# Kernel tuning notes

Measured on AMD Instinct MI355X. Metric: run time of the kernel, lower is better.

The kernel has to match this reference:

```python
import jax, jax.numpy as jnp
import numpy as np

N_NODES = 100000
N_EDGES = 1600000
D_IN = 128
D_HID = 128
N_CLASSES = 40


def _glorot(key, fan_in, fan_out):
    lim = np.sqrt(6.0 / (fan_in + fan_out)).astype(np.float32)
    return jax.random.uniform(key, (fan_in, fan_out), jnp.float32, -lim, lim)


def setup_inputs() -> dict:
    key = jax.random.key(0)
    ks = jax.random.split(key, 10)
    x = jax.random.normal(ks[0], (N_NODES, D_IN), jnp.float32)
    edge_index = jax.random.randint(ks[1], (2, N_EDGES), 0, N_NODES, jnp.int64)
    return {
        "x": x,
        "edge_index": edge_index,
        # layer 1: lin_l (neighbor, with bias), lin_r (root, no bias)
        "W1l": _glorot(ks[2], D_IN, D_HID),
        "b1": jnp.zeros((D_HID,), jnp.float32),
        "W1r": _glorot(ks[3], D_IN, D_HID),
        # layer 2
        "W2l": _glorot(ks[4], D_HID, D_HID),
        "b2": jnp.zeros((D_HID,), jnp.float32),
        "W2r": _glorot(ks[5], D_HID, D_HID),
        # layer 3
        "W3l": _glorot(ks[6], D_HID, N_CLASSES),
        "b3": jnp.zeros((N_CLASSES,), jnp.float32),
        "W3r": _glorot(ks[7], D_HID, N_CLASSES),
    }


def _sage_conv(x, src, dst, deg_inv, Wl, bl, Wr):
    # mean aggregation of source-node features onto destination nodes
    msgs = x[src]                                            # [E, d] gather
    agg = jax.ops.segment_sum(msgs, dst, num_segments=N_NODES)  # [N, d]
    agg = agg * deg_inv[:, None]                             # mean
    return agg @ Wl + bl + x @ Wr


def reference(x, edge_index, W1l, b1, W1r, W2l, b2, W2r, W3l, b3, W3r):
    src, dst = edge_index[0], edge_index[1]
    deg = jax.ops.segment_sum(jnp.ones((N_EDGES,), x.dtype), dst,
                              num_segments=N_NODES)
    deg_inv = 1.0 / jnp.maximum(deg, 1.0)
    h = _sage_conv(x, src, dst, deg_inv, W1l, b1, W1r)
    h = jax.nn.relu(h)  # dropout is identity in eval mode
    h = _sage_conv(h, src, dst, deg_inv, W2l, b2, W2r)
    h = jax.nn.relu(h)
    h = _sage_conv(h, src, dst, deg_inv, W3l, b3, W3r)
    return jax.nn.log_softmax(h, axis=1)
```

## Files before the change

kernel.cpp:

```cpp
#include <hip/hip_runtime.h>
#include <math.h>

#define D 128
#define NCLS 40
#define NBLK_P1 256

typedef unsigned int u32;
typedef __attribute__((ext_vector_type(8))) short short8;
typedef __attribute__((ext_vector_type(4))) float f32x4;

__device__ inline float bflo(u32 u){ return __uint_as_float(u << 16); }
__device__ inline float bfhi(u32 u){ return __uint_as_float(u & 0xffff0000u); }
__device__ inline u32 pack2bf(float a, float b){
  u32 ua = __float_as_uint(a), ub = __float_as_uint(b);
  ua += 0x7fffu + ((ua >> 16) & 1u);
  ub += 0x7fffu + ((ub >> 16) & 1u);
  return (ua >> 16) | (ub & 0xffff0000u);
}
__device__ inline unsigned short pack1bf(float a){
  u32 ua = __float_as_uint(a);
  ua += 0x7fffu + ((ua >> 16) & 1u);
  return (unsigned short)(ua >> 16);
}

__global__ __launch_bounds__(256) void prep_k(
    const float4* __restrict__ x4, uint2* __restrict__ xb, int n4,
    const float* __restrict__ W1l, const float* __restrict__ W1r, u32* __restrict__ Wt1,
    const float* __restrict__ W2l, const float* __restrict__ W2r, u32* __restrict__ Wt2,
    const float* __restrict__ W3l, const float* __restrict__ W3r,
    u32* __restrict__ Wt3b, float* __restrict__ bias3b, const float* __restrict__ b3,
    const int* __restrict__ dst, int* __restrict__ gcnt, int E, int nbuk, int nbX)
{
  __shared__ int cnt[1024];
  const int b = blockIdx.x;
  const int tid = threadIdx.x;
  if (b < nbX){
    int i = b * 256 + tid;
    if (i < n4){
      float4 v = x4[i];
      xb[i] = make_uint2(pack2bf(v.x, v.y), pack2bf(v.z, v.w));
    }
  } else if (b < nbX + 128){
    const bool first = (b < nbX + 64);
    const float* Wl = first ? W1l : W2l;
    const float* Wr = first ? W1r : W2r;
    u32* Wt = first ? Wt1 : Wt2;
    int i = ((b - nbX) & 63) * 256 + tid;
    int nn = i >> 7, kp = i & 127;
    int k = kp * 2;
    float a, c;
    if (k < 128){ a = Wl[(size_t)k * 128 + nn]; c = Wl[(size_t)(k + 1) * 128 + nn]; }
    else        { a = Wr[(size_t)(k - 128) * 128 + nn]; c = Wr[(size_t)(k - 127) * 128 + nn]; }
    Wt[(size_t)nn * 128 + kp] = pack2bf(a, c);
  } else if (b < nbX + 160){
    int i = (b - nbX - 128) * 256 + tid;
    if (i < 128 * 64){
      int nn = i >> 6, kp = i & 63;
      int k = kp * 2;
      float a = 0.f, c = 0.f;
      if (nn < NCLS){
        a = W3l[(size_t)k * NCLS + nn]; c = W3l[(size_t)(k + 1) * NCLS + nn];
      } else if (nn >= 64 && nn < 64 + NCLS){
        int cc = nn - 64;
        a = W3r[(size_t)k * NCLS + cc]; c = W3r[(size_t)(k + 1) * NCLS + cc];
      }
      Wt3b[(size_t)nn * 64 + kp] = pack2bf(a, c);
    }
    if (b == nbX + 128 && tid < 128)
      bias3b[tid] = (tid >= 64 && tid < 64 + NCLS) ? b3[tid - 64] : 0.f;
  } else {
    const int hb = b - nbX - 160;
    for (int i = tid; i < nbuk; i += 256) cnt[i] = 0;
    __syncthreads();
    const int per = (E + NBLK_P1 - 1) / NBLK_P1;
    const int e0 = hb * per;
    const int e1 = min(e0 + per, E);
    for (int i = e0 + tid; i < e1; i += 256)
      atomicAdd(&cnt[dst[i] >> 7], 1);
    __syncthreads();
    for (int i = tid; i < nbuk; i += 256)
      gcnt[(size_t)hb * nbuk + i] = cnt[i];
  }
}


__global__ __launch_bounds__(1024) void part_scan_k(
    const int* __restrict__ gcnt, int* __restrict__ goff,
    int* __restrict__ bbase, int nbuk)
{
  __shared__ int sm[1024];
  const int j = threadIdx.x;
  int btot = 0;
  if (j < nbuk)
    for (int i = 0; i < NBLK_P1; i++) btot += gcnt[(size_t)i * nbuk + j];
  sm[j] = btot;
  __syncthreads();
  int acc = btot;
  for (int off = 1; off < 1024; off <<= 1){
    int t = (j >= off) ? sm[j - off] : 0;
    __syncthreads();
    acc += t; sm[j] = acc;
    __syncthreads();
  }
  const int base = acc - btot;
  if (j < nbuk){
    bbase[j] = base;
    if (j == nbuk - 1) bbase[nbuk] = base + btot;
    int run = base;
    for (int i = 0; i < NBLK_P1; i++){
      goff[(size_t)i * nbuk + j] = run;
      run += gcnt[(size_t)i * nbuk + j];
    }
  }
}

__global__ __launch_bounds__(256) void part_fill_k(
    const int* __restrict__ src, const int* __restrict__ dst,
    const int* __restrict__ goff, u32* __restrict__ staging,
    int E, int nbuk)
{
  __shared__ int boff[1024];
  __shared__ int cur[1024];
  const int tid = threadIdx.x;
  for (int i = tid; i < nbuk; i += 256){
    boff[i] = goff[(size_t)blockIdx.x * nbuk + i];
    cur[i] = 0;
  }
  __syncthreads();
  const int per = (E + NBLK_P1 - 1) / NBLK_P1;
  const int e0 = blockIdx.x * per;
  const int e1 = min(e0 + per, E);
  for (int i = e0 + tid; i < e1; i += 256){
    int d = dst[i];
    int s = src[i];
    int b = d >> 7;
    int p = atomicAdd(&cur[b], 1);
    staging[boff[b] + p] = ((u32)s << 7) | (u32)(d & 127);
  }
}

__global__ __launch_bounds__(256) void bucket_csr_k(
    const u32* __restrict__ staging, const int* __restrict__ bbase,
    int* __restrict__ csr_off, float* __restrict__ deg_inv,
    int* __restrict__ csr_src, int N)
{
  __shared__ int ldeg[128];
  __shared__ int sm[128];
  __shared__ int lbase[128];
  __shared__ int lpos[128];
  const int b = blockIdx.x;
  const int node0 = b << 7;
  const int tid = threadIdx.x;
  if (tid < 128) ldeg[tid] = 0;
  __syncthreads();
  const int lo = bbase[b], hi = bbase[b + 1];
  for (int i = lo + tid; i < hi; i += 256)
    atomicAdd(&ldeg[staging[i] & 127u], 1);
  __syncthreads();
  if (tid < 128) sm[tid] = ldeg[tid];
  __syncthreads();
  for (int off = 1; off < 128; off <<= 1){
    int t = (tid >= off && tid < 128) ? sm[tid - off] : 0;
    __syncthreads();
    if (tid < 128) sm[tid] += t;
    __syncthreads();
  }
  if (tid < 128){
    const int excl = sm[tid] - ldeg[tid];
    lbase[tid] = lo + excl;
    lpos[tid] = 0;
    const int node = node0 + tid;
    if (node < N){
      csr_off[node] = lo + excl;
      deg_inv[node] = 1.0f / fmaxf((float)ldeg[tid], 1.0f);
    } else if (node == N){
      csr_off[N] = lo + excl;
    }
  }
  if (tid == 0 && b == (int)gridDim.x - 1) csr_off[N] = hi;
  __syncthreads();
  for (int i = lo + tid; i < hi; i += 256){
    u32 v = staging[i];
    int dloc = (int)(v & 127u);
    int p = atomicAdd(&lpos[dloc], 1);
    csr_src[lbase[dloc] + p] = (int)(v >> 7);
  }
}

__device__ inline void add8(float* acc, uint4 v){
  acc[0] += bflo(v.x); acc[1] += bfhi(v.x);
  acc[2] += bflo(v.y); acc[3] += bfhi(v.y);
  acc[4] += bflo(v.z); acc[5] += bfhi(v.z);
  acc[6] += bflo(v.w); acc[7] += bfhi(v.w);
}

__global__ __launch_bounds__(256) void aggregate_k(
    const u32* __restrict__ feat, const int* __restrict__ coff,
    const int* __restrict__ csr_src, const float* __restrict__ deg_inv,
    u32* __restrict__ agg, int n)
{
  const int g = threadIdx.x >> 4;
  const int lane = threadIdx.x & 15;
  const int node = blockIdx.x * 16 + g;
  if (node >= n) return;
  const int lo = coff[node], hi = coff[node + 1];
  const uint4* __restrict__ f4 = (const uint4*)feat;
  float acc[8] = {0.f,0.f,0.f,0.f,0.f,0.f,0.f,0.f};
  int e = lo;
  for (; e + 7 < hi; e += 8){
    int s0 = csr_src[e],     s1 = csr_src[e + 1];
    int s2 = csr_src[e + 2], s3 = csr_src[e + 3];
    int s4 = csr_src[e + 4], s5 = csr_src[e + 5];
    int s6 = csr_src[e + 6], s7 = csr_src[e + 7];
    uint4 v0 = f4[(size_t)s0 * 16 + lane];
    uint4 v1 = f4[(size_t)s1 * 16 + lane];
    uint4 v2 = f4[(size_t)s2 * 16 + lane];
    uint4 v3 = f4[(size_t)s3 * 16 + lane];
    uint4 v4 = f4[(size_t)s4 * 16 + lane];
    uint4 v5 = f4[(size_t)s5 * 16 + lane];
    uint4 v6 = f4[(size_t)s6 * 16 + lane];
    uint4 v7 = f4[(size_t)s7 * 16 + lane];
    add8(acc, v0); add8(acc, v1); add8(acc, v2); add8(acc, v3);
    add8(acc, v4); add8(acc, v5); add8(acc, v6); add8(acc, v7);
  }
  for (; e + 3 < hi; e += 4){
    int s0 = csr_src[e],     s1 = csr_src[e + 1];
    int s2 = csr_src[e + 2], s3 = csr_src[e + 3];
    uint4 v0 = f4[(size_t)s0 * 16 + lane];
    uint4 v1 = f4[(size_t)s1 * 16 + lane];
    uint4 v2 = f4[(size_t)s2 * 16 + lane];
    uint4 v3 = f4[(size_t)s3 * 16 + lane];
    add8(acc, v0); add8(acc, v1); add8(acc, v2); add8(acc, v3);
  }
  for (; e < hi; ++e){
    uint4 v0 = f4[(size_t)csr_src[e] * 16 + lane];
    add8(acc, v0);
  }
  const float di = deg_inv[node];
  uint4 o;
  o.x = pack2bf(acc[0] * di, acc[1] * di);
  o.y = pack2bf(acc[2] * di, acc[3] * di);
  o.z = pack2bf(acc[4] * di, acc[5] * di);
  o.w = pack2bf(acc[6] * di, acc[7] * di);
  ((uint4*)agg)[(size_t)node * 16 + lane] = o;
}

__global__ __launch_bounds__(256) void gemm_mfma_k(
    const u32* __restrict__ A1, const u32* __restrict__ A2,
    const u32* __restrict__ Wt, const float* __restrict__ bias,
    u32* __restrict__ out, int n)
{
  __shared__ u32 As_u[128 * 20];
  __shared__ u32 Bs_u[128 * 20];
  const int tid = threadIdx.x;
  const int row0 = blockIdx.x * 128;
  const int l = tid & 63, w = tid >> 6;
  const int lm = l & 15, lq = l >> 4;

  f32x4 acc[2][8];
  #pragma unroll
  for (int mi = 0; mi < 2; mi++)
    #pragma unroll
    for (int ni = 0; ni < 8; ni++) acc[mi][ni] = (f32x4){0.f, 0.f, 0.f, 0.f};

  for (int kt = 0; kt < 8; ++kt){
    const u32* Ap = (kt < 4) ? A1 : A2;
    const int ko = (kt & 3) * 16;
    #pragma unroll
    for (int i = 0; i < 2; i++){
      int chunk = tid + 256 * i;
      int row = chunk >> 2, q = chunk & 3;
      uint4 av = make_uint4(0, 0, 0, 0);
      int gr = row0 + row;
      if (gr < n) av = *(const uint4*)(Ap + (size_t)gr * 64 + ko + q * 4);
      *(uint4*)&As_u[row * 20 + q * 4] = av;
      uint4 bv = *(const uint4*)(Wt + (size_t)row * 128 + kt * 16 + q * 4);
      *(uint4*)&Bs_u[row * 20 + q * 4] = bv;
    }
    __syncthreads();
    short8 af0 = *(const short8*)&As_u[(w * 32 + lm) * 20 + lq * 4];
    short8 af1 = *(const short8*)&As_u[(w * 32 + 16 + lm) * 20 + lq * 4];
    #pragma unroll
    for (int ni = 0; ni < 8; ni++){
      short8 bf = *(const short8*)&Bs_u[(ni * 16 + lm) * 20 + lq * 4];
      acc[0][ni] = __builtin_amdgcn_mfma_f32_16x16x32_bf16(af0, bf, acc[0][ni], 0, 0, 0);
      acc[1][ni] = __builtin_amdgcn_mfma_f32_16x16x32_bf16(af1, bf, acc[1][ni], 0, 0, 0);
    }
    __syncthreads();
  }

  float bb[8];
  #pragma unroll
  for (int ni = 0; ni < 8; ni++) bb[ni] = bias[ni * 16 + lm];
  unsigned short* outp = (unsigned short*)out;
  #pragma unroll
  for (int mi = 0; mi < 2; mi++){
    #pragma unroll
    for (int r = 0; r < 4; r++){
      int row = row0 + w * 32 + mi * 16 + lq * 4 + r;
      if (row < n){
        #pragma unroll
        for (int ni = 0; ni < 8; ni++){
          float v = fmaxf(acc[mi][ni][r] + bb[ni], 0.f);
          outp[(size_t)row * 128 + ni * 16 + lm] = pack1bf(v);
        }
      }
    }
  }
}

__global__ __launch_bounds__(256) void gemm3_mfma_k(
    const u32* __restrict__ A, const u32* __restrict__ Wt3b,
    const float* __restrict__ bias, u32* __restrict__ out, int n)
{
  __shared__ u32 As_u[128 * 20];
  __shared__ u32 Bs_u[128 * 20];
  const int tid = threadIdx.x;
  const int row0 = blockIdx.x * 128;
  const int l = tid & 63, w = tid >> 6;
  const int lm = l & 15, lq = l >> 4;

  f32x4 acc[2][8];
  #pragma unroll
  for (int mi = 0; mi < 2; mi++)
    #pragma unroll
    for (int ni = 0; ni < 8; ni++) acc[mi][ni] = (f32x4){0.f, 0.f, 0.f, 0.f};

  for (int kt = 0; kt < 4; ++kt){
    #pragma unroll
    for (int i = 0; i < 2; i++){
      int chunk = tid + 256 * i;
      int row = chunk >> 2, q = chunk & 3;
      uint4 av = make_uint4(0, 0, 0, 0);
      int gr = row0 + row;
      if (gr < n) av = *(const uint4*)(A + (size_t)gr * 64 + kt * 16 + q * 4);
      *(uint4*)&As_u[row * 20 + q * 4] = av;
      uint4 bv = *(const uint4*)(Wt3b + (size_t)row * 64 + kt * 16 + q * 4);
      *(uint4*)&Bs_u[row * 20 + q * 4] = bv;
    }
    __syncthreads();
    short8 af0 = *(const short8*)&As_u[(w * 32 + lm) * 20 + lq * 4];
    short8 af1 = *(const short8*)&As_u[(w * 32 + 16 + lm) * 20 + lq * 4];
    #pragma unroll
    for (int ni = 0; ni < 8; ni++){
      short8 bf = *(const short8*)&Bs_u[(ni * 16 + lm) * 20 + lq * 4];
      acc[0][ni] = __builtin_amdgcn_mfma_f32_16x16x32_bf16(af0, bf, acc[0][ni], 0, 0, 0);
      acc[1][ni] = __builtin_amdgcn_mfma_f32_16x16x32_bf16(af1, bf, acc[1][ni], 0, 0, 0);
    }
    __syncthreads();
  }

  float bb[8];
  #pragma unroll
  for (int ni = 0; ni < 8; ni++) bb[ni] = bias[ni * 16 + lm];
  unsigned short* outp = (unsigned short*)out;
  #pragma unroll
  for (int mi = 0; mi < 2; mi++){
    #pragma unroll
    for (int r = 0; r < 4; r++){
      int row = row0 + w * 32 + mi * 16 + lq * 4 + r;
      if (row < n){
        #pragma unroll
        for (int ni = 0; ni < 8; ni++){
          float v = acc[mi][ni][r] + bb[ni];
          outp[(size_t)row * 128 + ni * 16 + lm] = pack1bf(v);
        }
      }
    }
  }
}

__global__ __launch_bounds__(256) void agg_softmax_k(
    const u32* __restrict__ yz, const int* __restrict__ coff,
    const int* __restrict__ csr_src, const float* __restrict__ deg_inv,
    float* __restrict__ out, int n)
{
  const int g = threadIdx.x >> 3;
  const int lane = threadIdx.x & 7;
  const int node = blockIdx.x * 32 + g;
  if (node >= n) return;
  const int lo = coff[node], hi = coff[node + 1];
  const uint4* __restrict__ f4 = (const uint4*)yz;
  float acc[8] = {0.f,0.f,0.f,0.f,0.f,0.f,0.f,0.f};
  int e = lo;
  for (; e + 7 < hi; e += 8){
    int s0 = csr_src[e],     s1 = csr_src[e + 1];
    int s2 = csr_src[e + 2], s3 = csr_src[e + 3];
    int s4 = csr_src[e + 4], s5 = csr_src[e + 5];
    int s6 = csr_src[e + 6], s7 = csr_src[e + 7];
    uint4 v0 = f4[(size_t)s0 * 16 + lane];
    uint4 v1 = f4[(size_t)s1 * 16 + lane];
    uint4 v2 = f4[(size_t)s2 * 16 + lane];
    uint4 v3 = f4[(size_t)s3 * 16 + lane];
    uint4 v4 = f4[(size_t)s4 * 16 + lane];
    uint4 v5 = f4[(size_t)s5 * 16 + lane];
    uint4 v6 = f4[(size_t)s6 * 16 + lane];
    uint4 v7 = f4[(size_t)s7 * 16 + lane];
    add8(acc, v0); add8(acc, v1); add8(acc, v2); add8(acc, v3);
    add8(acc, v4); add8(acc, v5); add8(acc, v6); add8(acc, v7);
  }
  for (; e + 3 < hi; e += 4){
    int s0 = csr_src[e],     s1 = csr_src[e + 1];
    int s2 = csr_src[e + 2], s3 = csr_src[e + 3];
    uint4 v0 = f4[(size_t)s0 * 16 + lane];
    uint4 v1 = f4[(size_t)s1 * 16 + lane];
    uint4 v2 = f4[(size_t)s2 * 16 + lane];
    uint4 v3 = f4[(size_t)s3 * 16 + lane];
    add8(acc, v0); add8(acc, v1); add8(acc, v2); add8(acc, v3);
  }
  for (; e < hi; ++e){
    uint4 v0 = f4[(size_t)csr_src[e] * 16 + lane];
    add8(acc, v0);
  }
  const float di = deg_inv[node];
  uint4 zv = f4[(size_t)node * 16 + 8 + lane];
  float v[8];
  v[0] = acc[0] * di + bflo(zv.x); v[1] = acc[1] * di + bfhi(zv.x);
  v[2] = acc[2] * di + bflo(zv.y); v[3] = acc[3] * di + bfhi(zv.y);
  v[4] = acc[4] * di + bflo(zv.z); v[5] = acc[5] * di + bfhi(zv.z);
  v[6] = acc[6] * di + bflo(zv.w); v[7] = acc[7] * di + bfhi(zv.w);
  const bool valid = (lane < 5);
  float m = -INFINITY;
  if (valid){
    #pragma unroll
    for (int j = 0; j < 8; j++) m = fmaxf(m, v[j]);
  }
  #pragma unroll
  for (int off = 1; off < 8; off <<= 1) m = fmaxf(m, __shfl_xor(m, off, 64));
  float s = 0.f;
  if (valid){
    #pragma unroll
    for (int j = 0; j < 8; j++) s += __expf(v[j] - m);
  }
  #pragma unroll
  for (int off = 1; off < 8; off <<= 1) s += __shfl_xor(s, off, 64);
  const float ls = m + logf(s);
  if (valid){
    float* op = out + (size_t)node * NCLS + lane * 8;
    *(float4*)op     = make_float4(v[0]-ls, v[1]-ls, v[2]-ls, v[3]-ls);
    *(float4*)(op+4) = make_float4(v[4]-ls, v[5]-ls, v[6]-ls, v[7]-ls);
  }
}


extern "C" void kernel_launch(void* const* d_in, const int* in_sizes, int n_in,
                              void* d_out, int out_size, void* d_ws, size_t ws_size,
                              hipStream_t stream) {
  const float* x   = (const float*)d_in[0];
  const int*   ei  = (const int*)d_in[1];
  const float* W1l = (const float*)d_in[2];
  const float* b1  = (const float*)d_in[3];
  const float* W1r = (const float*)d_in[4];
  const float* W2l = (const float*)d_in[5];
  const float* b2  = (const float*)d_in[6];
  const float* W2r = (const float*)d_in[7];
  const float* W3l = (const float*)d_in[8];
  const float* b3  = (const float*)d_in[9];
  const float* W3r = (const float*)d_in[10];

  const int N = in_sizes[0] / D;
  const int E = in_sizes[1] / 2;
  const int* src = ei;
  const int* dst = ei + E;
  const int nbuk = (N + 127) >> 7;

  char* ws = (char*)d_ws;
  auto alloc = [&](size_t bytes) -> void* {
    void* p = (void*)ws;
    ws += (bytes + 255) & ~(size_t)255;
    return p;
  };
  int*   csr_off  = (int*)  alloc((size_t)(N + 1) * 4);
  float* deg_inv  = (float*)alloc((size_t)N * 4);
  int*   csr_src  = (int*)  alloc((size_t)E * 4);
  u32*   staging  = (u32*)  alloc((size_t)E * 4);
  int*   gcnt     = (int*)  alloc((size_t)NBLK_P1 * nbuk * 4);
  int*   goff     = (int*)  alloc((size_t)NBLK_P1 * nbuk * 4);
  int*   bbase    = (int*)  alloc((size_t)(nbuk + 1) * 4);
  u32*   xb       = (u32*)  alloc((size_t)N * D * 2);
  u32*   agg      = (u32*)  alloc((size_t)N * D * 2);
  u32*   hbuf     = (u32*)  alloc((size_t)N * D * 2);
  u32*   yz       = (u32*)  alloc((size_t)N * D * 2);
  u32*   Wt1      = (u32*)  alloc((size_t)128 * 128 * 4);
  u32*   Wt2      = (u32*)  alloc((size_t)128 * 128 * 4);
  u32*   Wt3b    = (u32*)  alloc((size_t)128 * 64 * 4);
  float* bias3b   = (float*)alloc((size_t)128 * 4);

  const int n4 = N * D / 4;
  const int nbX = (n4 + 255) / 256;
  prep_k<<<nbX + 160 + NBLK_P1, 256, 0, stream>>>(
      (const float4*)x, (uint2*)xb, n4,
      W1l, W1r, Wt1, W2l, W2r, Wt2,
      W3l, W3r, Wt3b, bias3b, b3,
      dst, gcnt, E, nbuk, nbX);

  part_scan_k<<<1, 1024, 0, stream>>>(gcnt, goff, bbase, nbuk);
  part_fill_k<<<NBLK_P1, 256, 0, stream>>>(src, dst, goff, staging, E, nbuk);
  bucket_csr_k<<<nbuk, 256, 0, stream>>>(staging, bbase, csr_off, deg_inv, csr_src, N);

  const int gblocks = (N + 127) / 128;
  const int ablocks = (N + 15) / 16;
  aggregate_k<<<ablocks, 256, 0, stream>>>(xb, csr_off, csr_src, deg_inv, agg, N);
  gemm_mfma_k<<<gblocks, 256, 0, stream>>>(agg, xb, Wt1, b1, hbuf, N);
  aggregate_k<<<ablocks, 256, 0, stream>>>(hbuf, csr_off, csr_src, deg_inv, agg, N);
  gemm_mfma_k<<<gblocks, 256, 0, stream>>>(agg, hbuf, Wt2, b2, hbuf, N);
  gemm3_mfma_k<<<gblocks, 256, 0, stream>>>(hbuf, Wt3b, bias3b, yz, N);
  agg_softmax_k<<<(N + 31) / 32, 256, 0, stream>>>(yz, csr_off, csr_src, deg_inv,
                                                   (float*)d_out, N);
}
```

Before: 390.4 us.

## Store bf16 features column-chunked so gathers stay cache-resident per chunk

Features are stored in a chunk-major layout: eight 16-column bf16 chunks, each contiguous across all nodes. Aggregation kernels now process one chunk per block, so each pass gathers from a 3.2MB slab that can stay in cache instead of scattering across full 256B rows. Within a node, four lanes split the edges and are combined with shuffles. The final aggregate-plus-softmax is split into a chunked fp32 aggregation and a separate softmax kernel. The cost is an extra launch and an fp32 intermediate round trip, with more blocks each re-reading the CSR offsets and indices.

```diff
diff --git a/kernel.cpp b/kernel.cpp
--- a/kernel.cpp
+++ b/kernel.cpp
@@ -8,6 +8,7 @@
 typedef unsigned int u32;
 typedef __attribute__((ext_vector_type(8))) short short8;
 typedef __attribute__((ext_vector_type(4))) float f32x4;
+typedef __attribute__((ext_vector_type(4))) u32 u32x4;
 
 __device__ inline float bflo(u32 u){ return __uint_as_float(u << 16); }
 __device__ inline float bfhi(u32 u){ return __uint_as_float(u & 0xffff0000u); }
@@ -23,8 +24,9 @@
   return (unsigned short)(ua >> 16);
 }
 
+
 __global__ __launch_bounds__(256) void prep_k(
-    const float4* __restrict__ x4, uint2* __restrict__ xb, int n4,
+    const float4* __restrict__ x4, u32* __restrict__ xb, int n4,
     const float* __restrict__ W1l, const float* __restrict__ W1r, u32* __restrict__ Wt1,
     const float* __restrict__ W2l, const float* __restrict__ W2r, u32* __restrict__ Wt2,
     const float* __restrict__ W3l, const float* __restrict__ W3r,
@@ -37,8 +39,12 @@
   if (b < nbX){
     int i = b * 256 + tid;
     if (i < n4){
+      const int NN = n4 >> 5;
       float4 v = x4[i];
-      xb[i] = make_uint2(pack2bf(v.x, v.y), pack2bf(v.z, v.w));
+      int node = i >> 5;
+      int cu = (i * 2) & 63;
+      size_t idx = ((size_t)(cu >> 3) * NN + node) * 8 + (cu & 7);
+      *(uint2*)&xb[idx] = make_uint2(pack2bf(v.x, v.y), pack2bf(v.z, v.w));
     }
   } else if (b < nbX + 128){
     const bool first = (b < nbX + 64);
@@ -194,55 +200,48 @@
   acc[6] += bflo(v.w); acc[7] += bfhi(v.w);
 }
 
-__global__ __launch_bounds__(256) void aggregate_k(
+__global__ __launch_bounds__(256) void aggregate_c_k(
     const u32* __restrict__ feat, const int* __restrict__ coff,
     const int* __restrict__ csr_src, const float* __restrict__ deg_inv,
     u32* __restrict__ agg, int n)
 {
-  const int g = threadIdx.x >> 4;
-  const int lane = threadIdx.x & 15;
-  const int node = blockIdx.x * 16 + g;
+  const int c = blockIdx.x & 7;
+  const int g = threadIdx.x >> 3;
+  const int lane = threadIdx.x & 7;
+  const int node = (blockIdx.x >> 3) * 32 + g;
   if (node >= n) return;
+  const int h = lane & 1;
+  const int eslot = lane >> 1;
+  const uint4* __restrict__ Fc = (const uint4*)(feat + (size_t)c * n * 8);
   const int lo = coff[node], hi = coff[node + 1];
-  const uint4* __restrict__ f4 = (const uint4*)feat;
   float acc[8] = {0.f,0.f,0.f,0.f,0.f,0.f,0.f,0.f};
-  int e = lo;
-  for (; e + 7 < hi; e += 8){
-    int s0 = csr_src[e],     s1 = csr_src[e + 1];
-    int s2 = csr_src[e + 2], s3 = csr_src[e + 3];
-    int s4 = csr_src[e + 4], s5 = csr_src[e + 5];
-    int s6 = csr_src[e + 6], s7 = csr_src[e + 7];
-    uint4 v0 = f4[(size_t)s0 * 16 + lane];
-    uint4 v1 = f4[(size_t)s1 * 16 + lane];
-    uint4 v2 = f4[(size_t)s2 * 16 + lane];
-    uint4 v3 = f4[(size_t)s3 * 16 + lane];
-    uint4 v4 = f4[(size_t)s4 * 16 + lane];
-    uint4 v5 = f4[(size_t)s5 * 16 + lane];
-    uint4 v6 = f4[(size_t)s6 * 16 + lane];
-    uint4 v7 = f4[(size_t)s7 * 16 + lane];
-    add8(acc, v0); add8(acc, v1); add8(acc, v2); add8(acc, v3);
-    add8(acc, v4); add8(acc, v5); add8(acc, v6); add8(acc, v7);
-  }
-  for (; e + 3 < hi; e += 4){
-    int s0 = csr_src[e],     s1 = csr_src[e + 1];
-    int s2 = csr_src[e + 2], s3 = csr_src[e + 3];
-    uint4 v0 = f4[(size_t)s0 * 16 + lane];
-    uint4 v1 = f4[(size_t)s1 * 16 + lane];
-    uint4 v2 = f4[(size_t)s2 * 16 + lane];
-    uint4 v3 = f4[(size_t)s3 * 16 + lane];
-    add8(acc, v0); add8(acc, v1); add8(acc, v2); add8(acc, v3);
-  }
-  for (; e < hi; ++e){
-    uint4 v0 = f4[(size_t)csr_src[e] * 16 + lane];
+  int e = lo + eslot;
+  for (; e + 4 < hi; e += 8){
+    int s0 = __builtin_nontemporal_load(csr_src + e);
+    int s1 = __builtin_nontemporal_load(csr_src + e + 4);
+    uint4 v0 = Fc[(size_t)s0 * 2 + h];
+    uint4 v1 = Fc[(size_t)s1 * 2 + h];
+    add8(acc, v0); add8(acc, v1);
+  }
+  if (e < hi){
+    int s0 = __builtin_nontemporal_load(csr_src + e);
+    uint4 v0 = Fc[(size_t)s0 * 2 + h];
     add8(acc, v0);
   }
-  const float di = deg_inv[node];
-  uint4 o;
-  o.x = pack2bf(acc[0] * di, acc[1] * di);
-  o.y = pack2bf(acc[2] * di, acc[3] * di);
-  o.z = pack2bf(acc[4] * di, acc[5] * di);
-  o.w = pack2bf(acc[6] * di, acc[7] * di);
-  ((uint4*)agg)[(size_t)node * 16 + lane] = o;
+  #pragma unroll
+  for (int off = 2; off <= 4; off <<= 1)
+    #pragma unroll
+    for (int j = 0; j < 8; j++)
+      acc[j] += __shfl_xor(acc[j], off, 64);
+  if (eslot == 0){
+    const float di = deg_inv[node];
+    u32x4 o;
+    o.x = pack2bf(acc[0] * di, acc[1] * di);
+    o.y = pack2bf(acc[2] * di, acc[3] * di);
+    o.z = pack2bf(acc[4] * di, acc[5] * di);
+    o.w = pack2bf(acc[6] * di, acc[7] * di);
+    __builtin_nontemporal_store(o, (u32x4*)(agg + ((size_t)c * n + node) * 8 + h * 4));
+  }
 }
 
 __global__ __launch_bounds__(256) void gemm_mfma_k(
@@ -272,7 +271,8 @@
       int row = chunk >> 2, q = chunk & 3;
       uint4 av = make_uint4(0, 0, 0, 0);
       int gr = row0 + row;
-      if (gr < n) av = *(const uint4*)(Ap + (size_t)gr * 64 + ko + q * 4);
+      int cu = ko + q * 4;
+      if (gr < n) av = *(const uint4*)(Ap + ((size_t)(cu >> 3) * n + gr) * 8 + (cu & 7));
       *(uint4*)&As_u[row * 20 + q * 4] = av;
       uint4 bv = *(const uint4*)(Wt + (size_t)row * 128 + kt * 16 + q * 4);
       *(uint4*)&Bs_u[row * 20 + q * 4] = bv;
@@ -302,7 +302,7 @@
         #pragma unroll
         for (int ni = 0; ni < 8; ni++){
           float v = fmaxf(acc[mi][ni][r] + bb[ni], 0.f);
-          outp[(size_t)row * 128 + ni * 16 + lm] = pack1bf(v);
+          outp[((size_t)ni * n + row) * 16 + lm] = pack1bf(v);
         }
       }
     }
@@ -333,7 +333,8 @@
       int row = chunk >> 2, q = chunk & 3;
       uint4 av = make_uint4(0, 0, 0, 0);
       int gr = row0 + row;
-      if (gr < n) av = *(const uint4*)(A + (size_t)gr * 64 + kt * 16 + q * 4);
+      int cu = kt * 16 + q * 4;
+      if (gr < n) av = *(const uint4*)(A + ((size_t)(cu >> 3) * n + gr) * 8 + (cu & 7));
       *(uint4*)&As_u[row * 20 + q * 4] = av;
       uint4 bv = *(const uint4*)(Wt3b + (size_t)row * 64 + kt * 16 + q * 4);
       *(uint4*)&Bs_u[row * 20 + q * 4] = bv;
@@ -363,62 +364,74 @@
         #pragma unroll
         for (int ni = 0; ni < 8; ni++){
           float v = acc[mi][ni][r] + bb[ni];
-          outp[(size_t)row * 128 + ni * 16 + lm] = pack1bf(v);
+          outp[((size_t)ni * n + row) * 16 + lm] = pack1bf(v);
         }
       }
     }
   }
 }
 
-__global__ __launch_bounds__(256) void agg_softmax_k(
+__global__ __launch_bounds__(256) void yagg_c_k(
     const u32* __restrict__ yz, const int* __restrict__ coff,
     const int* __restrict__ csr_src, const float* __restrict__ deg_inv,
+    float* __restrict__ yagg, int n)
+{
+  const int c = blockIdx.x & 3;
+  const int g = threadIdx.x >> 3;
+  const int lane = threadIdx.x & 7;
+  const int node = (blockIdx.x >> 2) * 32 + g;
+  if (node >= n) return;
+  const int h = lane & 1;
+  const int eslot = lane >> 1;
+  const uint4* __restrict__ Fc = (const uint4*)(yz + (size_t)c * n * 8);
+  const int lo = coff[node], hi = coff[node + 1];
+  float acc[8] = {0.f,0.f,0.f,0.f,0.f,0.f,0.f,0.f};
+  int e = lo + eslot;
+  for (; e + 4 < hi; e += 8){
+    int s0 = __builtin_nontemporal_load(csr_src + e);
+    int s1 = __builtin_nontemporal_load(csr_src + e + 4);
+    uint4 v0 = Fc[(size_t)s0 * 2 + h];
+    uint4 v1 = Fc[(size_t)s1 * 2 + h];
+    add8(acc, v0); add8(acc, v1);
+  }
+  if (e < hi){
+    int s0 = __builtin_nontemporal_load(csr_src + e);
+    uint4 v0 = Fc[(size_t)s0 * 2 + h];
+    add8(acc, v0);
+  }
+  #pragma unroll
+  for (int off = 2; off <= 4; off <<= 1)
+    #pragma unroll
+    for (int j = 0; j < 8; j++)
+      acc[j] += __shfl_xor(acc[j], off, 64);
+  if (eslot == 0){
+    const float di = deg_inv[node];
+    float* yp = yagg + ((size_t)c * n + node) * 16 + h * 8;
+    f32x4 o0 = (f32x4){acc[0]*di, acc[1]*di, acc[2]*di, acc[3]*di};
+    f32x4 o1 = (f32x4){acc[4]*di, acc[5]*di, acc[6]*di, acc[7]*di};
+    __builtin_nontemporal_store(o0, (f32x4*)yp);
+    __builtin_nontemporal_store(o1, (f32x4*)(yp + 4));
+  }
+}
+
+__global__ __launch_bounds__(256) void softmax_k(
+    const float* __restrict__ yagg, const u32* __restrict__ yz,
     float* __restrict__ out, int n)
 {
   const int g = threadIdx.x >> 3;
   const int lane = threadIdx.x & 7;
   const int node = blockIdx.x * 32 + g;
   if (node >= n) return;
-  const int lo = coff[node], hi = coff[node + 1];
-  const uint4* __restrict__ f4 = (const uint4*)yz;
-  float acc[8] = {0.f,0.f,0.f,0.f,0.f,0.f,0.f,0.f};
-  int e = lo;
-  for (; e + 7 < hi; e += 8){
-    int s0 = csr_src[e],     s1 = csr_src[e + 1];
-    int s2 = csr_src[e + 2], s3 = csr_src[e + 3];
-    int s4 = csr_src[e + 4], s5 = csr_src[e + 5];
-    int s6 = csr_src[e + 6], s7 = csr_src[e + 7];
-    uint4 v0 = f4[(size_t)s0 * 16 + lane];
-    uint4 v1 = f4[(size_t)s1 * 16 + lane];
-    uint4 v2 = f4[(size_t)s2 * 16 + lane];
-    uint4 v3 = f4[(size_t)s3 * 16 + lane];
-    uint4 v4 = f4[(size_t)s4 * 16 + lane];
-    uint4 v5 = f4[(size_t)s5 * 16 + lane];
-    uint4 v6 = f4[(size_t)s6 * 16 + lane];
-    uint4 v7 = f4[(size_t)s7 * 16 + lane];
-    add8(acc, v0); add8(acc, v1); add8(acc, v2); add8(acc, v3);
-    add8(acc, v4); add8(acc, v5); add8(acc, v6); add8(acc, v7);
-  }
-  for (; e + 3 < hi; e += 4){
-    int s0 = csr_src[e],     s1 = csr_src[e + 1];
-    int s2 = csr_src[e + 2], s3 = csr_src[e + 3];
-    uint4 v0 = f4[(size_t)s0 * 16 + lane];
-    uint4 v1 = f4[(size_t)s1 * 16 + lane];
-    uint4 v2 = f4[(size_t)s2 * 16 + lane];
-    uint4 v3 = f4[(size_t)s3 * 16 + lane];
-    add8(acc, v0); add8(acc, v1); add8(acc, v2); add8(acc, v3);
-  }
-  for (; e < hi; ++e){
-    uint4 v0 = f4[(size_t)csr_src[e] * 16 + lane];
-    add8(acc, v0);
-  }
-  const float di = deg_inv[node];
-  uint4 zv = f4[(size_t)node * 16 + 8 + lane];
+  const float4* yp = (const float4*)(yagg + ((size_t)(lane >> 1) * n + node) * 16
+                                     + (lane & 1) * 8);
+  float4 a0 = yp[0], a1 = yp[1];
+  const uint4 zv = *(const uint4*)(yz + ((size_t)(4 + (lane >> 1)) * n + node) * 8
+                                   + (lane & 1) * 4);
   float v[8];
-  v[0] = acc[0] * di + bflo(zv.x); v[1] = acc[1] * di + bfhi(zv.x);
-  v[2] = acc[2] * di + bflo(zv.y); v[3] = acc[3] * di + bfhi(zv.y);
-  v[4] = acc[4] * di + bflo(zv.z); v[5] = acc[5] * di + bfhi(zv.z);
-  v[6] = acc[6] * di + bflo(zv.w); v[7] = acc[7] * di + bfhi(zv.w);
+  v[0] = a0.x + bflo(zv.x); v[1] = a0.y + bfhi(zv.x);
+  v[2] = a0.z + bflo(zv.y); v[3] = a0.w + bfhi(zv.y);
+  v[4] = a1.x + bflo(zv.z); v[5] = a1.y + bfhi(zv.z);
+  v[6] = a1.z + bflo(zv.w); v[7] = a1.w + bfhi(zv.w);
   const bool valid = (lane < 5);
   float m = -INFINITY;
   if (valid){
@@ -483,13 +496,14 @@
   u32*   yz       = (u32*)  alloc((size_t)N * D * 2);
   u32*   Wt1      = (u32*)  alloc((size_t)128 * 128 * 4);
   u32*   Wt2      = (u32*)  alloc((size_t)128 * 128 * 4);
-  u32*   Wt3b    = (u32*)  alloc((size_t)128 * 64 * 4);
+  u32*   Wt3b     = (u32*)  alloc((size_t)128 * 64 * 4);
   float* bias3b   = (float*)alloc((size_t)128 * 4);
+  float* yagg     = (float*)agg;
 
   const int n4 = N * D / 4;
   const int nbX = (n4 + 255) / 256;
   prep_k<<<nbX + 160 + NBLK_P1, 256, 0, stream>>>(
-      (const float4*)x, (uint2*)xb, n4,
+      (const float4*)x, xb, n4,
       W1l, W1r, Wt1, W2l, W2r, Wt2,
       W3l, W3r, Wt3b, bias3b, b3,
       dst, gcnt, E, nbuk, nbX);
@@ -499,12 +513,12 @@
   bucket_csr_k<<<nbuk, 256, 0, stream>>>(staging, bbase, csr_off, deg_inv, csr_src, N);
 
   const int gblocks = (N + 127) / 128;
-  const int ablocks = (N + 15) / 16;
-  aggregate_k<<<ablocks, 256, 0, stream>>>(xb, csr_off, csr_src, deg_inv, agg, N);
+  const int nb32 = (N + 31) / 32;
+  aggregate_c_k<<<8 * nb32, 256, 0, stream>>>(xb, csr_off, csr_src, deg_inv, agg, N);
   gemm_mfma_k<<<gblocks, 256, 0, stream>>>(agg, xb, Wt1, b1, hbuf, N);
-  aggregate_k<<<ablocks, 256, 0, stream>>>(hbuf, csr_off, csr_src, deg_inv, agg, N);
+  aggregate_c_k<<<8 * nb32, 256, 0, stream>>>(hbuf, csr_off, csr_src, deg_inv, agg, N);
   gemm_mfma_k<<<gblocks, 256, 0, stream>>>(agg, hbuf, Wt2, b2, hbuf, N);
   gemm3_mfma_k<<<gblocks, 256, 0, stream>>>(hbuf, Wt3b, bias3b, yz, N);
-  agg_softmax_k<<<(N + 31) / 32, 256, 0, stream>>>(yz, csr_off, csr_src, deg_inv,
-                                                   (float*)d_out, N);
-}
+  yagg_c_k<<<4 * nb32, 256, 0, stream>>>(yz, csr_off, csr_src, deg_inv, yagg, N);
+  softmax_k<<<nb32, 256, 0, stream>>>(yagg, yz, (float*)d_out, N);
+}
```

After: 560.1 us. 1.43x slower.

## Parallelize partition scan across blocks and stage GEMM outputs for coalesced stores

Applied to the files above, without the earlier changes.

The single-block partition scan, which looped serially over 256 per-block counts for each bucket, is split into three kernels: a per-bucket reduction, a single-block scan of the bucket totals, and a per-bucket block-offset scan. This spreads the serial work across many blocks at the cost of two extra launches. Separately, both MFMA GEMM kernels now write their bf16 results into shared memory first and then emit 16-byte vector stores per row, replacing scattered 2-byte global stores. This enlarges shared memory per block, which may reduce occupancy.

```diff
diff --git a/kernel.cpp b/kernel.cpp
--- a/kernel.cpp
+++ b/kernel.cpp
@@ -84,34 +84,59 @@
 }
 
 
-__global__ __launch_bounds__(1024) void part_scan_k(
-    const int* __restrict__ gcnt, int* __restrict__ goff,
-    int* __restrict__ bbase, int nbuk)
+__global__ __launch_bounds__(256) void bsum_k(
+    const int* __restrict__ gcnt, int* __restrict__ btot, int nbuk)
+{
+  __shared__ int sm[256];
+  const int j = blockIdx.x;
+  sm[threadIdx.x] = gcnt[(size_t)threadIdx.x * nbuk + j];
+  __syncthreads();
+  for (int off = 128; off > 0; off >>= 1){
+    if (threadIdx.x < off) sm[threadIdx.x] += sm[threadIdx.x + off];
+    __syncthreads();
+  }
+  if (threadIdx.x == 0) btot[j] = sm[0];
+}
+
+__global__ __launch_bounds__(1024) void scan_k(
+    const int* __restrict__ btot, int* __restrict__ bbase, int nbuk)
 {
   __shared__ int sm[1024];
   const int j = threadIdx.x;
-  int btot = 0;
-  if (j < nbuk)
-    for (int i = 0; i < NBLK_P1; i++) btot += gcnt[(size_t)i * nbuk + j];
-  sm[j] = btot;
-  __syncthreads();
-  int acc = btot;
+  int v = (j < nbuk) ? btot[j] : 0;
+  sm[j] = v;
+  __syncthreads();
+  int acc = v;
   for (int off = 1; off < 1024; off <<= 1){
     int t = (j >= off) ? sm[j - off] : 0;
     __syncthreads();
     acc += t; sm[j] = acc;
     __syncthreads();
   }
-  const int base = acc - btot;
   if (j < nbuk){
-    bbase[j] = base;
-    if (j == nbuk - 1) bbase[nbuk] = base + btot;
-    int run = base;
-    for (int i = 0; i < NBLK_P1; i++){
-      goff[(size_t)i * nbuk + j] = run;
-      run += gcnt[(size_t)i * nbuk + j];
-    }
-  }
+    bbase[j] = acc - v;
+    if (j == nbuk - 1) bbase[nbuk] = acc;
+  }
+}
+
+__global__ __launch_bounds__(256) void goff_k(
+    const int* __restrict__ gcnt, const int* __restrict__ bbase,
+    int* __restrict__ goff, int nbuk)
+{
+  __shared__ int sm[256];
+  const int j = blockIdx.x;
+  const int i = threadIdx.x;
+  int v = gcnt[(size_t)i * nbuk + j];
+  sm[i] = v;
+  __syncthreads();
+  int acc = v;
+  for (int off = 1; off < 256; off <<= 1){
+    int t = (i >= off) ? sm[i - off] : 0;
+    __syncthreads();
+    acc += t; sm[i] = acc;
+    __syncthreads();
+  }
+  goff[(size_t)i * nbuk + j] = bbase[j] + acc - v;
 }
 
 __global__ __launch_bounds__(256) void part_fill_k(
@@ -250,8 +275,9 @@
     const u32* __restrict__ Wt, const float* __restrict__ bias,
     u32* __restrict__ out, int n)
 {
-  __shared__ u32 As_u[128 * 20];
-  __shared__ u32 Bs_u[128 * 20];
+  __shared__ u32 smem[8704];
+  u32* As_u = smem;
+  u32* Bs_u = smem + 2560;
   const int tid = threadIdx.x;
   const int row0 = blockIdx.x * 128;
   const int l = tid & 63, w = tid >> 6;
@@ -292,20 +318,28 @@
   float bb[8];
   #pragma unroll
   for (int ni = 0; ni < 8; ni++) bb[ni] = bias[ni * 16 + lm];
-  unsigned short* outp = (unsigned short*)out;
-  #pragma unroll
-  for (int mi = 0; mi < 2; mi++){
+  unsigned short* es = (unsigned short*)smem + w * (32 * 136);
+  #pragma unroll
+  for (int mi = 0; mi < 2; mi++)
     #pragma unroll
     for (int r = 0; r < 4; r++){
-      int row = row0 + w * 32 + mi * 16 + lq * 4 + r;
-      if (row < n){
-        #pragma unroll
-        for (int ni = 0; ni < 8; ni++){
-          float v = fmaxf(acc[mi][ni][r] + bb[ni], 0.f);
-          outp[(size_t)row * 128 + ni * 16 + lm] = pack1bf(v);
-        }
+      const int Lr = mi * 16 + lq * 4 + r;
+      #pragma unroll
+      for (int ni = 0; ni < 8; ni++){
+        float v = fmaxf(acc[mi][ni][r] + bb[ni], 0.f);
+        es[Lr * 136 + ni * 16 + lm] = pack1bf(v);
       }
     }
+  __syncthreads();
+  uint4* outv = (uint4*)out;
+  const int cl = l & 15;
+  const int rsub = l >> 4;
+  #pragma unroll
+  for (int p = 0; p < 8; p++){
+    const int Lr = p * 4 + rsub;
+    const int row = row0 + w * 32 + Lr;
+    uint4 t = *(const uint4*)&es[Lr * 136 + cl * 8];
+    if (row < n) outv[(size_t)row * 16 + cl] = t;
   }
 }
 
@@ -313,8 +347,9 @@
     const u32* __restrict__ A, const u32* __restrict__ Wt3b,
     const float* __restrict__ bias, u32* __restrict__ out, int n)
 {
-  __shared__ u32 As_u[128 * 20];
-  __shared__ u32 Bs_u[128 * 20];
+  __shared__ u32 smem[8704];
+  u32* As_u = smem;
+  u32* Bs_u = smem + 2560;
   const int tid = threadIdx.x;
   const int row0 = blockIdx.x * 128;
   const int l = tid & 63, w = tid >> 6;
@@ -353,20 +388,28 @@
   float bb[8];
   #pragma unroll
   for (int ni = 0; ni < 8; ni++) bb[ni] = bias[ni * 16 + lm];
-  unsigned short* outp = (unsigned short*)out;
-  #pragma unroll
-  for (int mi = 0; mi < 2; mi++){
+  unsigned short* es = (unsigned short*)smem + w * (32 * 136);
+  #pragma unroll
+  for (int mi = 0; mi < 2; mi++)
     #pragma unroll
     for (int r = 0; r < 4; r++){
-      int row = row0 + w * 32 + mi * 16 + lq * 4 + r;
-      if (row < n){
-        #pragma unroll
-        for (int ni = 0; ni < 8; ni++){
-          float v = acc[mi][ni][r] + bb[ni];
-          outp[(size_t)row * 128 + ni * 16 + lm] = pack1bf(v);
-        }
+      const int Lr = mi * 16 + lq * 4 + r;
+      #pragma unroll
+      for (int ni = 0; ni < 8; ni++){
+        float v = acc[mi][ni][r] + bb[ni];
+        es[Lr * 136 + ni * 16 + lm] = pack1bf(v);
       }
     }
+  __syncthreads();
+  uint4* outv = (uint4*)out;
+  const int cl = l & 15;
+  const int rsub = l >> 4;
+  #pragma unroll
+  for (int p = 0; p < 8; p++){
+    const int Lr = p * 4 + rsub;
+    const int row = row0 + w * 32 + Lr;
+    uint4 t = *(const uint4*)&es[Lr * 136 + cl * 8];
+    if (row < n) outv[(size_t)row * 16 + cl] = t;
   }
 }
 
@@ -477,6 +520,7 @@
   int*   gcnt     = (int*)  alloc((size_t)NBLK_P1 * nbuk * 4);
   int*   goff     = (int*)  alloc((size_t)NBLK_P1 * nbuk * 4);
   int*   bbase    = (int*)  alloc((size_t)(nbuk + 1) * 4);
+  int*   btot     = (int*)  alloc((size_t)(nbuk + 1) * 4);
   u32*   xb       = (u32*)  alloc((size_t)N * D * 2);
   u32*   agg      = (u32*)  alloc((size_t)N * D * 2);
   u32*   hbuf     = (u32*)  alloc((size_t)N * D * 2);
@@ -494,7 +538,9 @@
       W3l, W3r, Wt3b, bias3b, b3,
       dst, gcnt, E, nbuk, nbX);
 
-  part_scan_k<<<1, 1024, 0, stream>>>(gcnt, goff, bbase, nbuk);
+  bsum_k<<<nbuk, 256, 0, stream>>>(gcnt, btot, nbuk);
+  scan_k<<<1, 1024, 0, stream>>>(btot, bbase, nbuk);
+  goff_k<<<nbuk, 256, 0, stream>>>(gcnt, bbase, goff, nbuk);
   part_fill_k<<<NBLK_P1, 256, 0, stream>>>(src, dst, goff, staging, E, nbuk);
   bucket_csr_k<<<nbuk, 256, 0, stream>>>(staging, bbase, csr_off, deg_inv, csr_src, N);
 
```

After: 385.0 us. About the same (-1.4%).
